# Optimization experiments

Measured on AMD Instinct MI355X. Metric: run time of the kernel, lower is better.

## Reference

```python
import jax, jax.numpy as jnp
import numpy as np

D = 256
H = 16
HD = D // H
N_BIAS = 6
B, E = 8, 1024


def _layernorm(x, g, b, eps=1e-5):
    mu = jnp.mean(x, axis=-1, keepdims=True)
    var = jnp.mean(jnp.square(x - mu), axis=-1, keepdims=True)
    return (x - mu) * jax.lax.rsqrt(var + eps) * g + b


def setup_inputs() -> dict:
    key = jax.random.key(0)
    ks = jax.random.split(key, 16)
    s = 0.02
    inp = {
        "x": jax.random.normal(ks[0], (B, E, D), dtype=jnp.float32),
        "struct_bias": jax.random.randint(ks[1], (B, E, E), 0, N_BIAS),
        "key_padding_mask": jnp.zeros((B, E), dtype=bool),
        # projections stored as [in, out] so y = x @ W + b
        "Wq": jax.random.normal(ks[2], (D, D), jnp.float32) * s,
        "bq": jnp.zeros((D,), jnp.float32),
        "Wk": jax.random.normal(ks[3], (D, D), jnp.float32) * s,
        "bk": jnp.zeros((D,), jnp.float32),
        "Wv": jax.random.normal(ks[4], (D, D), jnp.float32) * s,
        "bv": jnp.zeros((D,), jnp.float32),
        "Wo": jax.random.normal(ks[5], (D, D), jnp.float32) * s,
        "bo": jnp.zeros((D,), jnp.float32),
        "bias_emb": jax.random.normal(ks[6], (N_BIAS, H), jnp.float32) * s,
        "ln1_g": jnp.ones((D,), jnp.float32),
        "ln1_b": jnp.zeros((D,), jnp.float32),
        "W_ff1": jax.random.normal(ks[7], (D, 4 * D), jnp.float32) * s,
        "b_ff1": jnp.zeros((4 * D,), jnp.float32),
        "W_ff2": jax.random.normal(ks[8], (4 * D, D), jnp.float32) * s,
        "b_ff2": jnp.zeros((D,), jnp.float32),
        "ln2_g": jnp.ones((D,), jnp.float32),
        "ln2_b": jnp.zeros((D,), jnp.float32),
    }
    return inp


def reference(x, struct_bias, key_padding_mask, Wq, bq, Wk, bk, Wv, bv, Wo, bo,
              bias_emb, ln1_g, ln1_b, W_ff1, b_ff1, W_ff2, b_ff2, ln2_g, ln2_b):
    b, e, d = x.shape
    # project and split heads: [B, H, E, HD]
    q = (x @ Wq + bq).reshape(b, e, H, HD).transpose(0, 2, 1, 3)
    k = (x @ Wk + bk).reshape(b, e, H, HD).transpose(0, 2, 1, 3)
    v = (x @ Wv + bv).reshape(b, e, H, HD).transpose(0, 2, 1, 3)
    scores = jnp.einsum('bhqd,bhkd->bhqk', q, k) / np.sqrt(HD).astype(np.float32)
    # learned structural bias: [B,E,E,H] -> [B,H,E,E]
    bias = bias_emb[struct_bias].transpose(0, 3, 1, 2)
    scores = scores + bias
    scores = jnp.where(key_padding_mask[:, None, None, :], -jnp.inf, scores)
    attn = jax.nn.softmax(scores, axis=-1)
    out = jnp.einsum('bhqk,bhkd->bhqd', attn, v)
    out = out.transpose(0, 2, 1, 3).reshape(b, e, d)
    out = out @ Wo + bo
    x = _layernorm(x + out, ln1_g, ln1_b)
    ff = jax.nn.gelu(x @ W_ff1 + b_ff1, approximate=False) @ W_ff2 + b_ff2
    x = _layernorm(x + ff, ln2_g, ln2_b)
    return x
```

## Files before the change

### kernel.cpp

```cpp
#include <hip/hip_runtime.h>
#include <math.h>

#define B_  8
#define E_  1024
#define D_  256
#define H_  16
#define FF_ 1024
#define M_  (B_ * E_)

typedef __attribute__((ext_vector_type(8))) short short8;
typedef __attribute__((ext_vector_type(4))) float f32x4;
typedef unsigned short bf16u;

#define GLOAD_LDS16(g, l) __builtin_amdgcn_global_load_lds( \
    (const __attribute__((address_space(1))) void*)(g), \
    (__attribute__((address_space(3))) void*)(l), 16, 0, 0)

__device__ __forceinline__ unsigned short f2bf(float f) {
  union { float f; unsigned u; } c; c.f = f;
  unsigned r = c.u + 0x7fffu + ((c.u >> 16) & 1u);
  return (unsigned short)(r >> 16);
}
__device__ __forceinline__ float gelu_exact(float x) {
  return 0.5f * x * (1.0f + erff(x * 0.70710678118654752f));
}

template<int BM, int BN, int EPI>
__global__ __launch_bounds__(256) void mm_k(
    const bf16u* __restrict__ A, const bf16u* __restrict__ Wt,
    const float* __restrict__ bias, const float* __restrict__ R,
    void* __restrict__ Cout, int M, int N, int K)
{
  constexpr int WM = BM / 2, WN = BN / 2;
  constexpr int MT = WM / 16, NT = WN / 16;
  constexpr int PA = BM * 8 / 256, PB = BN * 8 / 256;
  constexpr int LBM = (BM == 128 ? 7 : 6), LBN = (BN == 128 ? 7 : 6);
  __shared__ bf16u As[BM * 64];
  __shared__ bf16u Bs[BN * 64];

  const int t = threadIdx.x;
  const int l15 = t & 15, quad = (t >> 4) & 3;
  const int w = t >> 6, wm = w >> 1, wn = w & 1;
  const int m0 = blockIdx.x * BM, n0 = blockIdx.y * BN;

  f32x4 acc[MT][NT];
  const f32x4 z4 = {0.f, 0.f, 0.f, 0.f};
#pragma unroll
  for (int i = 0; i < MT; ++i)
#pragma unroll
    for (int j = 0; j < NT; ++j) acc[i][j] = z4;

  for (int k0 = 0; k0 < K; k0 += 64) {
    __syncthreads();
#pragma unroll
    for (int p = 0; p < PA; ++p) {
      int g = p * 256 + t;
      int m = g & (BM - 1), c = g >> LBM;
      const bf16u* src = A + (size_t)(m0 + m) * K + k0 + c * 8;
      GLOAD_LDS16(src, As + g * 8);
    }
#pragma unroll
    for (int p = 0; p < PB; ++p) {
      int g = p * 256 + t;
      int n = g & (BN - 1), c = g >> LBN;
      const bf16u* src = Wt + (size_t)(n0 + n) * K + k0 + c * 8;
      GLOAD_LDS16(src, Bs + g * 8);
    }
    __syncthreads();
#pragma unroll
    for (int s = 0; s < 2; ++s) {
      short8 af[MT], bfr[NT];
#pragma unroll
      for (int mt = 0; mt < MT; ++mt)
        af[mt] = *(const short8*)(As + ((s * 4 + quad) * BM + wm * WM + mt * 16 + l15) * 8);
#pragma unroll
      for (int nt = 0; nt < NT; ++nt)
        bfr[nt] = *(const short8*)(Bs + ((s * 4 + quad) * BN + wn * WN + nt * 16 + l15) * 8);
#pragma unroll
      for (int mt = 0; mt < MT; ++mt)
#pragma unroll
        for (int nt = 0; nt < NT; ++nt)
          acc[mt][nt] = __builtin_amdgcn_mfma_f32_16x16x32_bf16(
              af[mt], bfr[nt], acc[mt][nt], 0, 0, 0);
    }
  }

#pragma unroll
  for (int mt = 0; mt < MT; ++mt) {
#pragma unroll
    for (int nt = 0; nt < NT; ++nt) {
      int col = n0 + wn * WN + nt * 16 + l15;
      float bia = bias[col];
#pragma unroll
      for (int r = 0; r < 4; ++r) {
        int row = m0 + wm * WM + mt * 16 + quad * 4 + r;
        size_t idx = (size_t)row * N + col;
        float v = acc[mt][nt][r] + bia;
        if (EPI == 1)      { ((float*)Cout)[idx] = v + R[idx]; }
        else if (EPI == 2) { ((bf16u*)Cout)[idx] = f2bf(gelu_exact(v)); }
        else               { ((bf16u*)Cout)[idx] = f2bf(v); }
      }
    }
  }
}

__global__ __launch_bounds__(256) void tcvt4_k(
    const float* __restrict__ s0, const float* __restrict__ s1,
    const float* __restrict__ s2, const float* __restrict__ s3,
    bf16u* __restrict__ d0, bf16u* __restrict__ d1,
    bf16u* __restrict__ d2, bf16u* __restrict__ d3)
{
  const int z = blockIdx.z;
  const float* src = (z == 0) ? s0 : (z == 1) ? s1 : (z == 2) ? s2 : s3;
  bf16u* dst = (z == 0) ? d0 : (z == 1) ? d1 : (z == 2) ? d2 : d3;
  __shared__ float tile[32][33];
  const int tx = threadIdx.x & 31, ty = threadIdx.x >> 5;
  const int kb = blockIdx.x * 32, nb = blockIdx.y * 32;
#pragma unroll
  for (int r = 0; r < 4; ++r)
    tile[ty + 8 * r][tx] = src[(size_t)(kb + ty + 8 * r) * 256 + nb + tx];
  __syncthreads();
#pragma unroll
  for (int r = 0; r < 4; ++r)
    dst[(size_t)(nb + ty + 8 * r) * 256 + kb + tx] = f2bf(tile[tx][ty + 8 * r]);
}

__global__ __launch_bounds__(256) void tcvt_k(const float* __restrict__ src,
    bf16u* __restrict__ dst, int K, int N)
{
  __shared__ float tile[32][33];
  const int tx = threadIdx.x & 31, ty = threadIdx.x >> 5;
  const int kb = blockIdx.x * 32, nb = blockIdx.y * 32;
#pragma unroll
  for (int r = 0; r < 4; ++r)
    tile[ty + 8 * r][tx] = src[(size_t)(kb + ty + 8 * r) * N + nb + tx];
  __syncthreads();
#pragma unroll
  for (int r = 0; r < 4; ++r)
    dst[(size_t)(nb + ty + 8 * r) * K + kb + tx] = f2bf(tile[tx][ty + 8 * r]);
}

__global__ __launch_bounds__(256) void cvt_k(const float* __restrict__ X,
    bf16u* __restrict__ Y)
{
  int i = blockIdx.x * 256 + threadIdx.x;
  float4 a = ((const float4*)X)[i * 2];
  float4 b = ((const float4*)X)[i * 2 + 1];
  uint4 o;
  o.x = f2bf(a.x) | ((unsigned)f2bf(a.y) << 16);
  o.y = f2bf(a.z) | ((unsigned)f2bf(a.w) << 16);
  o.z = f2bf(b.x) | ((unsigned)f2bf(b.y) << 16);
  o.w = f2bf(b.z) | ((unsigned)f2bf(b.w) << 16);
  ((uint4*)Y)[i] = o;
}

__global__ void bcat_k(const float* __restrict__ bq, const float* __restrict__ bk,
                       const float* __restrict__ bv, float* __restrict__ o)
{
  int i = blockIdx.x * 256 + threadIdx.x;
  o[i] = (i < 256) ? bq[i] : (i < 512) ? bk[i - 256] : bv[i - 512];
}

__global__ __launch_bounds__(256) void attn_k(
    const bf16u* __restrict__ qkv, const int* __restrict__ sb,
    const unsigned char* __restrict__ mask, const float* __restrict__ be,
    bf16u* __restrict__ O)
{
  __shared__ bf16u Kl[2][64][40];
  __shared__ bf16u Vt[2][16][72];
  __shared__ bf16u Pl[4][16][40];
  __shared__ float embl[2][6];

  const int t    = threadIdx.x;
  const int b    = blockIdx.z;
  const int hg   = blockIdx.y;
  const int w    = t >> 6;
  const int lane = t & 63;
  const int l15  = lane & 15;
  const int quad = lane >> 4;
  const int q0w  = blockIdx.x * 64 + w * 16;

  if (t < 12) embl[t / 6][t % 6] = be[(t % 6) * 16 + hg * 2 + t / 6];

  {
    float4 z = {0.f, 0.f, 0.f, 0.f};
    float4* kp = (float4*)&Kl[0][0][0];
    for (int i = t; i < 640; i += 256) kp[i] = z;
  }

  short8 qf[2];
#pragma unroll
  for (int hp = 0; hp < 2; ++hp) {
    uint4 v = {0u, 0u, 0u, 0u};
    if (quad < 2)
      v = *(const uint4*)(qkv + ((size_t)(b * E_) + q0w + l15) * 768 +
                          (hg * 2 + hp) * 16 + quad * 8);
    else if (quad == 2)
      v.x = 0x3F80u;
    union { uint4 u; short8 s; } c; c.u = v;
    qf[hp] = c.s;
  }

  const int s_hp   = t >> 7;
  const int s_key  = (t >> 1) & 63;
  const int s_half = t & 1;
  const size_t kvbase = (size_t)b * E_ * 768;
  const int* sbp = sb + ((size_t)b * E_ + q0w) * E_;

  f32x4 accO[2];
  const f32x4 z4 = {0.f, 0.f, 0.f, 0.f};
  accO[0] = z4; accO[1] = z4;
  float lsum[2][4] = {};

  for (int k0 = 0; k0 < E_; k0 += 64) {
    int sbv[2][2][4];
#pragma unroll
    for (int s2 = 0; s2 < 2; ++s2)
#pragma unroll
      for (int f = 0; f < 2; ++f)
#pragma unroll
        for (int r = 0; r < 4; ++r)
          sbv[s2][f][r] = sbp[(size_t)(quad * 4 + r) * E_ + k0 + s2 * 32 + f * 16 + l15];

    __syncthreads();
    {
      const bf16u* kq = qkv + kvbase + (size_t)(k0 + s_key) * 768 + 256 +
                        (hg * 2 + s_hp) * 16 + s_half * 8;
      uint4 kw = *(const uint4*)kq;
      uint4 vw = *(const uint4*)(kq + 256);
      *(uint4*)&Kl[s_hp][s_key][s_half * 8] = kw;
      const int col = (s_key >> 5) * 32 + ((s_key & 15) << 1) + ((s_key >> 4) & 1);
      union { uint4 u; bf16u e[8]; } vc; vc.u = vw;
#pragma unroll
      for (int j = 0; j < 8; ++j)
        Vt[s_hp][s_half * 8 + j][col] = vc.e[j];
      if (s_half == 0) {
        unsigned char mv = mask[b * E_ + k0 + s_key];
        Kl[s_hp][s_key][16] = mv ? (bf16u)0xCF6E : (bf16u)0;
      }
    }
    __syncthreads();

#pragma unroll
    for (int hp = 0; hp < 2; ++hp) {
#pragma unroll
      for (int s2 = 0; s2 < 2; ++s2) {
        short8 kf0 = *(const short8*)&Kl[hp][s2 * 32 + l15][quad * 8];
        short8 kf1 = *(const short8*)&Kl[hp][s2 * 32 + 16 + l15][quad * 8];
        f32x4 sc0 = __builtin_amdgcn_mfma_f32_16x16x32_bf16(qf[hp], kf0, z4, 0, 0, 0);
        f32x4 sc1 = __builtin_amdgcn_mfma_f32_16x16x32_bf16(qf[hp], kf1, z4, 0, 0, 0);
#pragma unroll
        for (int r = 0; r < 4; ++r) {
          float w0 = embl[hp][sbv[s2][0][r]];
          float w1 = embl[hp][sbv[s2][1][r]];
          float p0 = __expf(fmaf(sc0[r], 0.25f, w0));
          float p1 = __expf(fmaf(sc1[r], 0.25f, w1));
          unsigned u0 = __float_as_uint(p0) & 0xffff0000u;
          unsigned u1 = __float_as_uint(p1) & 0xffff0000u;
          lsum[hp][r] += __uint_as_float(u0) + __uint_as_float(u1);
          *(unsigned*)&Pl[w][quad * 4 + r][l15 * 2] = (__float_as_uint(p0) >> 16) | u1;
        }
        short8 pf = *(const short8*)&Pl[w][l15][quad * 8];
        short8 vf = *(const short8*)&Vt[hp][l15][s2 * 32 + quad * 8];
        accO[hp] = __builtin_amdgcn_mfma_f32_16x16x32_bf16(pf, vf, accO[hp], 0, 0, 0);
      }
    }
  }

#pragma unroll
  for (int off = 1; off <= 8; off <<= 1)
#pragma unroll
    for (int hp = 0; hp < 2; ++hp)
#pragma unroll
      for (int r = 0; r < 4; ++r)
        lsum[hp][r] += __shfl_xor(lsum[hp][r], off, 64);

#pragma unroll
  for (int hp = 0; hp < 2; ++hp) {
#pragma unroll
    for (int r = 0; r < 4; ++r) {
      float o = accO[hp][r] / lsum[hp][r];
      O[((size_t)(b * E_) + q0w + quad * 4 + r) * 256 + (hg * 2 + hp) * 16 + l15] = f2bf(o);
    }
  }
}

template<int DUAL>
__global__ __launch_bounds__(256) void ln_k(
    const float* __restrict__ X, const float* __restrict__ g,
    const float* __restrict__ bta, float* __restrict__ Y, bf16u* __restrict__ Yb)
{
  const int row  = blockIdx.x * 4 + (threadIdx.x >> 6);
  const int lane = threadIdx.x & 63;
  float4 v = *(const float4*)(X + (size_t)row * D_ + lane * 4);
  float s  = v.x + v.y + v.z + v.w;
  float ss = v.x * v.x + v.y * v.y + v.z * v.z + v.w * v.w;
#pragma unroll
  for (int off = 32; off; off >>= 1) {
    s  += __shfl_xor(s, off, 64);
    ss += __shfl_xor(ss, off, 64);
  }
  float mu  = s * (1.f / 256.f);
  float var = ss * (1.f / 256.f) - mu * mu;
  float rs  = 1.f / sqrtf(var + 1e-5f);
  float4 gv = *(const float4*)(g + lane * 4);
  float4 bv = *(const float4*)(bta + lane * 4);
  float4 o;
  o.x = (v.x - mu) * rs * gv.x + bv.x;
  o.y = (v.y - mu) * rs * gv.y + bv.y;
  o.z = (v.z - mu) * rs * gv.z + bv.z;
  o.w = (v.w - mu) * rs * gv.w + bv.w;
  *(float4*)(Y + (size_t)row * D_ + lane * 4) = o;
  if (DUAL) {
    uint2 p;
    p.x = f2bf(o.x) | ((unsigned)f2bf(o.y) << 16);
    p.y = f2bf(o.z) | ((unsigned)f2bf(o.w) << 16);
    *(uint2*)(Yb + (size_t)row * D_ + lane * 4) = p;
  }
}

extern "C" void kernel_launch(void* const* d_in, const int* in_sizes, int n_in,
                              void* d_out, int out_size, void* d_ws, size_t ws_size,
                              hipStream_t stream) {
  const float* x   = (const float*)d_in[0];
  const int*   sb  = (const int*)d_in[1];
  const unsigned char* mask = (const unsigned char*)d_in[2];
  const float* Wq  = (const float*)d_in[3];
  const float* bq  = (const float*)d_in[4];
  const float* Wk  = (const float*)d_in[5];
  const float* bk  = (const float*)d_in[6];
  const float* Wv  = (const float*)d_in[7];
  const float* bv  = (const float*)d_in[8];
  const float* Wo  = (const float*)d_in[9];
  const float* bo  = (const float*)d_in[10];
  const float* be  = (const float*)d_in[11];
  const float* g1  = (const float*)d_in[12];
  const float* b1  = (const float*)d_in[13];
  const float* Wf1 = (const float*)d_in[14];
  const float* bf1 = (const float*)d_in[15];
  const float* Wf2 = (const float*)d_in[16];
  const float* bf2 = (const float*)d_in[17];
  const float* g2  = (const float*)d_in[18];
  const float* b2  = (const float*)d_in[19];
  float* out = (float*)d_out;

  char* ws = (char*)d_ws;
  bf16u* Wqkvt = (bf16u*)(ws + 0);
  bf16u* Wot   = (bf16u*)(ws + 393216);
  bf16u* Wf1t  = (bf16u*)(ws + 524288);
  bf16u* Wf2t  = (bf16u*)(ws + 1048576);
  float* bqkv  = (float*)(ws + 1572864);
  bf16u* xb    = (bf16u*)(ws + 2097152);
  bf16u* qkv   = (bf16u*)(ws + 6291456);
  bf16u* att   = (bf16u*)(ws + 18874368);
  float* t1    = (float*)(ws + 23068672);
  float* x1    = (float*)(ws + 31457280);
  bf16u* x1b   = (bf16u*)(ws + 39845888);
  bf16u* ffh   = (bf16u*)(ws + 2097152);
  float* t2    = (float*)(ws + 18874368);

  dim3 blk(256);

  tcvt4_k<<<dim3(8, 8, 4), blk, 0, stream>>>(Wq, Wk, Wv, Wo,
      Wqkvt, Wqkvt + 65536, Wqkvt + 131072, Wot);
  tcvt_k<<<dim3(8, 32), blk, 0, stream>>>(Wf1, Wf1t, 256, 1024);
  tcvt_k<<<dim3(32, 8), blk, 0, stream>>>(Wf2, Wf2t, 1024, 256);
  bcat_k<<<3, blk, 0, stream>>>(bq, bk, bv, bqkv);
  cvt_k<<<1024, blk, 0, stream>>>(x, xb);

  mm_k<128, 128, 0><<<dim3(64, 6), blk, 0, stream>>>(xb, Wqkvt, bqkv, nullptr,
                                                     qkv, M_, 768, 256);
  attn_k<<<dim3(16, 8, 8), blk, 0, stream>>>(qkv, sb, mask, be, att);

  mm_k<64, 64, 1><<<dim3(128, 4), blk, 0, stream>>>(att, Wot, bo, x,
                                                    t1, M_, 256, 256);
  ln_k<1><<<M_ / 4, blk, 0, stream>>>(t1, g1, b1, x1, x1b);

  mm_k<128, 128, 2><<<dim3(64, 8), blk, 0, stream>>>(x1b, Wf1t, bf1, nullptr,
                                                     ffh, M_, 1024, 256);
  mm_k<64, 64, 1><<<dim3(128, 4), blk, 0, stream>>>(ffh, Wf2t, bf2, x1,
                                                    t2, M_, 256, 1024);
  ln_k<0><<<M_ / 4, blk, 0, stream>>>(t2, g2, b2, out, nullptr);
}
```

Baseline: 239.5 us.

## Fuse residual+LayerNorm into output GEMMs and merge prep kernels into one launch

Adds a GEMM kernel that computes a full 32-row by 256-column output tile per block, adds bias and residual, and does LayerNorm in the epilogue with a cross-wave reduction in LDS. It replaces the Wo and FF2 GEMMs plus their separate LayerNorm passes, removing the fp32 intermediate round trips and two launches. The five weight, bias and input conversion kernels are also merged into a single prep launch. The fused GEMM uses only 256 blocks with a large B tile and no double-buffering, so it may lose parallelism and latency hiding compared with the previous 512-block GEMMs.

```diff
diff --git a/kernel.cpp b/kernel.cpp
--- a/kernel.cpp
+++ b/kernel.cpp
@@ -96,69 +96,198 @@
         int row = m0 + wm * WM + mt * 16 + quad * 4 + r;
         size_t idx = (size_t)row * N + col;
         float v = acc[mt][nt][r] + bia;
-        if (EPI == 1)      { ((float*)Cout)[idx] = v + R[idx]; }
-        else if (EPI == 2) { ((bf16u*)Cout)[idx] = f2bf(gelu_exact(v)); }
-        else               { ((bf16u*)Cout)[idx] = f2bf(v); }
-      }
-    }
-  }
-}
-
-__global__ __launch_bounds__(256) void tcvt4_k(
-    const float* __restrict__ s0, const float* __restrict__ s1,
-    const float* __restrict__ s2, const float* __restrict__ s3,
-    bf16u* __restrict__ d0, bf16u* __restrict__ d1,
-    bf16u* __restrict__ d2, bf16u* __restrict__ d3)
+        if (EPI == 2) { ((bf16u*)Cout)[idx] = f2bf(gelu_exact(v)); }
+        else          { ((bf16u*)Cout)[idx] = f2bf(v); }
+      }
+    }
+  }
+}
+
+template<int K_, int LN1>
+__global__ __launch_bounds__(256) void mm_ln_k(
+    const bf16u* __restrict__ A, const bf16u* __restrict__ Wt,
+    const float* __restrict__ bias, const float* __restrict__ R,
+    const float* __restrict__ gam, const float* __restrict__ bet,
+    float* __restrict__ Yf, bf16u* __restrict__ Yb)
 {
-  const int z = blockIdx.z;
-  const float* src = (z == 0) ? s0 : (z == 1) ? s1 : (z == 2) ? s2 : s3;
-  bf16u* dst = (z == 0) ? d0 : (z == 1) ? d1 : (z == 2) ? d2 : d3;
-  __shared__ float tile[32][33];
-  const int tx = threadIdx.x & 31, ty = threadIdx.x >> 5;
-  const int kb = blockIdx.x * 32, nb = blockIdx.y * 32;
-#pragma unroll
-  for (int r = 0; r < 4; ++r)
-    tile[ty + 8 * r][tx] = src[(size_t)(kb + ty + 8 * r) * 256 + nb + tx];
+  __shared__ bf16u As[32 * 64];
+  __shared__ bf16u Bs[256 * 64];
+  __shared__ float red[2][32][4];
+
+  const int t = threadIdx.x;
+  const int l15 = t & 15, quad = (t >> 4) & 3;
+  const int w = t >> 6;
+  const int m0 = blockIdx.x * 32;
+
+  f32x4 acc[2][4];
+  const f32x4 z4 = {0.f, 0.f, 0.f, 0.f};
+#pragma unroll
+  for (int i = 0; i < 2; ++i)
+#pragma unroll
+    for (int j = 0; j < 4; ++j) acc[i][j] = z4;
+
+  for (int k0 = 0; k0 < K_; k0 += 64) {
+    __syncthreads();
+    {
+      const bf16u* src = A + (size_t)(m0 + (t & 31)) * K_ + k0 + (t >> 5) * 8;
+      GLOAD_LDS16(src, As + t * 8);
+    }
+#pragma unroll
+    for (int p = 0; p < 8; ++p) {
+      int g = p * 256 + t;
+      const bf16u* src = Wt + (size_t)(g & 255) * K_ + k0 + (g >> 8) * 8;
+      GLOAD_LDS16(src, Bs + g * 8);
+    }
+    __syncthreads();
+#pragma unroll
+    for (int s = 0; s < 2; ++s) {
+      const int cc = s * 4 + quad;
+      short8 af[2], bfr[4];
+#pragma unroll
+      for (int mt = 0; mt < 2; ++mt)
+        af[mt] = *(const short8*)(As + (cc * 32 + mt * 16 + l15) * 8);
+#pragma unroll
+      for (int nt = 0; nt < 4; ++nt)
+        bfr[nt] = *(const short8*)(Bs + (cc * 256 + w * 64 + nt * 16 + l15) * 8);
+#pragma unroll
+      for (int mt = 0; mt < 2; ++mt)
+#pragma unroll
+        for (int nt = 0; nt < 4; ++nt)
+          acc[mt][nt] = __builtin_amdgcn_mfma_f32_16x16x32_bf16(
+              af[mt], bfr[nt], acc[mt][nt], 0, 0, 0);
+    }
+  }
+
+  float ga[4], be4[4], bi[4];
+#pragma unroll
+  for (int nt = 0; nt < 4; ++nt) {
+    int col = w * 64 + nt * 16 + l15;
+    bi[nt] = bias[col]; ga[nt] = gam[col]; be4[nt] = bet[col];
+  }
+#pragma unroll
+  for (int mt = 0; mt < 2; ++mt)
+#pragma unroll
+    for (int nt = 0; nt < 4; ++nt) {
+      int col = w * 64 + nt * 16 + l15;
+#pragma unroll
+      for (int r = 0; r < 4; ++r) {
+        int row = m0 + mt * 16 + quad * 4 + r;
+        acc[mt][nt][r] += bi[nt] + R[(size_t)row * 256 + col];
+      }
+    }
+
+  float s1[2][4], s2[2][4];
+#pragma unroll
+  for (int mt = 0; mt < 2; ++mt)
+#pragma unroll
+    for (int r = 0; r < 4; ++r) {
+      float a = 0.f, b = 0.f;
+#pragma unroll
+      for (int nt = 0; nt < 4; ++nt) {
+        float v = acc[mt][nt][r];
+        a += v; b += v * v;
+      }
+      s1[mt][r] = a; s2[mt][r] = b;
+    }
+#pragma unroll
+  for (int off = 1; off <= 8; off <<= 1)
+#pragma unroll
+    for (int mt = 0; mt < 2; ++mt)
+#pragma unroll
+      for (int r = 0; r < 4; ++r) {
+        s1[mt][r] += __shfl_xor(s1[mt][r], off, 64);
+        s2[mt][r] += __shfl_xor(s2[mt][r], off, 64);
+      }
+  if (l15 == 0) {
+#pragma unroll
+    for (int mt = 0; mt < 2; ++mt)
+#pragma unroll
+      for (int r = 0; r < 4; ++r) {
+        int row32 = mt * 16 + quad * 4 + r;
+        red[0][row32][w] = s1[mt][r];
+        red[1][row32][w] = s2[mt][r];
+      }
+  }
   __syncthreads();
-#pragma unroll
-  for (int r = 0; r < 4; ++r)
-    dst[(size_t)(nb + ty + 8 * r) * 256 + kb + tx] = f2bf(tile[tx][ty + 8 * r]);
-}
-
-__global__ __launch_bounds__(256) void tcvt_k(const float* __restrict__ src,
-    bf16u* __restrict__ dst, int K, int N)
+
+#pragma unroll
+  for (int mt = 0; mt < 2; ++mt)
+#pragma unroll
+    for (int r = 0; r < 4; ++r) {
+      int row32 = mt * 16 + quad * 4 + r;
+      float4 sa = *(const float4*)&red[0][row32][0];
+      float4 sb = *(const float4*)&red[1][row32][0];
+      float sum = sa.x + sa.y + sa.z + sa.w;
+      float sq  = sb.x + sb.y + sb.z + sb.w;
+      float mu  = sum * (1.f / 256.f);
+      float var = sq * (1.f / 256.f) - mu * mu;
+      float rs  = 1.f / sqrtf(var + 1e-5f);
+      int row = m0 + row32;
+#pragma unroll
+      for (int nt = 0; nt < 4; ++nt) {
+        int col = w * 64 + nt * 16 + l15;
+        float y = (acc[mt][nt][r] - mu) * rs * ga[nt] + be4[nt];
+        size_t idx = (size_t)row * 256 + col;
+        Yf[idx] = y;
+        if (LN1) Yb[idx] = f2bf(y);
+      }
+    }
+}
+
+__global__ __launch_bounds__(256) void prep_k(
+    const float* __restrict__ x, bf16u* __restrict__ xb,
+    const float* __restrict__ Wq, const float* __restrict__ Wk,
+    const float* __restrict__ Wv, const float* __restrict__ Wo,
+    bf16u* __restrict__ Wqkvt, bf16u* __restrict__ Wot,
+    const float* __restrict__ Wf1, bf16u* __restrict__ Wf1t,
+    const float* __restrict__ Wf2, bf16u* __restrict__ Wf2t,
+    const float* __restrict__ bq, const float* __restrict__ bk,
+    const float* __restrict__ bv, float* __restrict__ bqkv)
 {
   __shared__ float tile[32][33];
-  const int tx = threadIdx.x & 31, ty = threadIdx.x >> 5;
-  const int kb = blockIdx.x * 32, nb = blockIdx.y * 32;
-#pragma unroll
-  for (int r = 0; r < 4; ++r)
-    tile[ty + 8 * r][tx] = src[(size_t)(kb + ty + 8 * r) * N + nb + tx];
-  __syncthreads();
-#pragma unroll
-  for (int r = 0; r < 4; ++r)
-    dst[(size_t)(nb + ty + 8 * r) * K + kb + tx] = f2bf(tile[tx][ty + 8 * r]);
-}
-
-__global__ __launch_bounds__(256) void cvt_k(const float* __restrict__ X,
-    bf16u* __restrict__ Y)
-{
-  int i = blockIdx.x * 256 + threadIdx.x;
-  float4 a = ((const float4*)X)[i * 2];
-  float4 b = ((const float4*)X)[i * 2 + 1];
-  uint4 o;
-  o.x = f2bf(a.x) | ((unsigned)f2bf(a.y) << 16);
-  o.y = f2bf(a.z) | ((unsigned)f2bf(a.w) << 16);
-  o.z = f2bf(b.x) | ((unsigned)f2bf(b.y) << 16);
-  o.w = f2bf(b.z) | ((unsigned)f2bf(b.w) << 16);
-  ((uint4*)Y)[i] = o;
-}
-
-__global__ void bcat_k(const float* __restrict__ bq, const float* __restrict__ bk,
-                       const float* __restrict__ bv, float* __restrict__ o)
-{
-  int i = blockIdx.x * 256 + threadIdx.x;
-  o[i] = (i < 256) ? bq[i] : (i < 512) ? bk[i - 256] : bv[i - 512];
+  const int bid = blockIdx.x;
+  const int t = threadIdx.x;
+
+  if (bid < 1024) {
+    int i = bid * 256 + t;
+    float4 a = ((const float4*)x)[i * 2];
+    float4 b = ((const float4*)x)[i * 2 + 1];
+    uint4 o;
+    o.x = f2bf(a.x) | ((unsigned)f2bf(a.y) << 16);
+    o.y = f2bf(a.z) | ((unsigned)f2bf(a.w) << 16);
+    o.z = f2bf(b.x) | ((unsigned)f2bf(b.y) << 16);
+    o.w = f2bf(b.z) | ((unsigned)f2bf(b.w) << 16);
+    ((uint4*)xb)[i] = o;
+  } else if (bid < 1792) {
+    const float* src; bf16u* dst; int K, N, kb, nb;
+    int rr = bid - 1024;
+    if (rr < 256) {
+      int z = rr >> 6, i = rr & 63;
+      src = (z == 0) ? Wq : (z == 1) ? Wk : (z == 2) ? Wv : Wo;
+      dst = (z == 0) ? Wqkvt : (z == 1) ? Wqkvt + 65536
+          : (z == 2) ? Wqkvt + 131072 : Wot;
+      K = 256; N = 256; kb = (i & 7) * 32; nb = (i >> 3) * 32;
+    } else if (rr < 512) {
+      int i = rr - 256;
+      src = Wf1; dst = Wf1t; K = 256; N = 1024;
+      kb = (i & 7) * 32; nb = (i >> 3) * 32;
+    } else {
+      int i = rr - 512;
+      src = Wf2; dst = Wf2t; K = 1024; N = 256;
+      kb = (i & 31) * 32; nb = (i >> 5) * 32;
+    }
+    const int tx = t & 31, ty = t >> 5;
+#pragma unroll
+    for (int r = 0; r < 4; ++r)
+      tile[ty + 8 * r][tx] = src[(size_t)(kb + ty + 8 * r) * N + nb + tx];
+    __syncthreads();
+#pragma unroll
+    for (int r = 0; r < 4; ++r)
+      dst[(size_t)(nb + ty + 8 * r) * K + kb + tx] = f2bf(tile[tx][ty + 8 * r]);
+  } else {
+    for (int i = t; i < 768; i += 256)
+      bqkv[i] = (i < 256) ? bq[i] : (i < 512) ? bk[i - 256] : bv[i - 512];
+  }
 }
 
 __global__ __launch_bounds__(256) void attn_k(
@@ -282,40 +411,6 @@
       float o = accO[hp][r] / lsum[hp][r];
       O[((size_t)(b * E_) + q0w + quad * 4 + r) * 256 + (hg * 2 + hp) * 16 + l15] = f2bf(o);
     }
-  }
-}
-
-template<int DUAL>
-__global__ __launch_bounds__(256) void ln_k(
-    const float* __restrict__ X, const float* __restrict__ g,
-    const float* __restrict__ bta, float* __restrict__ Y, bf16u* __restrict__ Yb)
-{
-  const int row  = blockIdx.x * 4 + (threadIdx.x >> 6);
-  const int lane = threadIdx.x & 63;
-  float4 v = *(const float4*)(X + (size_t)row * D_ + lane * 4);
-  float s  = v.x + v.y + v.z + v.w;
-  float ss = v.x * v.x + v.y * v.y + v.z * v.z + v.w * v.w;
-#pragma unroll
-  for (int off = 32; off; off >>= 1) {
-    s  += __shfl_xor(s, off, 64);
-    ss += __shfl_xor(ss, off, 64);
-  }
-  float mu  = s * (1.f / 256.f);
-  float var = ss * (1.f / 256.f) - mu * mu;
-  float rs  = 1.f / sqrtf(var + 1e-5f);
-  float4 gv = *(const float4*)(g + lane * 4);
-  float4 bv = *(const float4*)(bta + lane * 4);
-  float4 o;
-  o.x = (v.x - mu) * rs * gv.x + bv.x;
-  o.y = (v.y - mu) * rs * gv.y + bv.y;
-  o.z = (v.z - mu) * rs * gv.z + bv.z;
-  o.w = (v.w - mu) * rs * gv.w + bv.w;
-  *(float4*)(Y + (size_t)row * D_ + lane * 4) = o;
-  if (DUAL) {
-    uint2 p;
-    p.x = f2bf(o.x) | ((unsigned)f2bf(o.y) << 16);
-    p.y = f2bf(o.z) | ((unsigned)f2bf(o.w) << 16);
-    *(uint2*)(Yb + (size_t)row * D_ + lane * 4) = p;
   }
 }
 
@@ -353,32 +448,22 @@
   bf16u* xb    = (bf16u*)(ws + 2097152);
   bf16u* qkv   = (bf16u*)(ws + 6291456);
   bf16u* att   = (bf16u*)(ws + 18874368);
-  float* t1    = (float*)(ws + 23068672);
-  float* x1    = (float*)(ws + 31457280);
-  bf16u* x1b   = (bf16u*)(ws + 39845888);
+  float* x1    = (float*)(ws + 23068672);
+  bf16u* x1b   = (bf16u*)(ws + 31457280);
   bf16u* ffh   = (bf16u*)(ws + 2097152);
-  float* t2    = (float*)(ws + 18874368);
 
   dim3 blk(256);
 
-  tcvt4_k<<<dim3(8, 8, 4), blk, 0, stream>>>(Wq, Wk, Wv, Wo,
-      Wqkvt, Wqkvt + 65536, Wqkvt + 131072, Wot);
-  tcvt_k<<<dim3(8, 32), blk, 0, stream>>>(Wf1, Wf1t, 256, 1024);
-  tcvt_k<<<dim3(32, 8), blk, 0, stream>>>(Wf2, Wf2t, 1024, 256);
-  bcat_k<<<3, blk, 0, stream>>>(bq, bk, bv, bqkv);
-  cvt_k<<<1024, blk, 0, stream>>>(x, xb);
+  prep_k<<<1793, blk, 0, stream>>>(x, xb, Wq, Wk, Wv, Wo, Wqkvt, Wot,
+                                   Wf1, Wf1t, Wf2, Wf2t, bq, bk, bv, bqkv);
 
   mm_k<128, 128, 0><<<dim3(64, 6), blk, 0, stream>>>(xb, Wqkvt, bqkv, nullptr,
                                                      qkv, M_, 768, 256);
   attn_k<<<dim3(16, 8, 8), blk, 0, stream>>>(qkv, sb, mask, be, att);
 
-  mm_k<64, 64, 1><<<dim3(128, 4), blk, 0, stream>>>(att, Wot, bo, x,
-                                                    t1, M_, 256, 256);
-  ln_k<1><<<M_ / 4, blk, 0, stream>>>(t1, g1, b1, x1, x1b);
+  mm_ln_k<256, 1><<<256, blk, 0, stream>>>(att, Wot, bo, x, g1, b1, x1, x1b);
 
   mm_k<128, 128, 2><<<dim3(64, 8), blk, 0, stream>>>(x1b, Wf1t, bf1, nullptr,
                                                      ffh, M_, 1024, 256);
-  mm_k<64, 64, 1><<<dim3(128, 4), blk, 0, stream>>>(ffh, Wf2t, bf2, x1,
-                                                    t2, M_, 256, 1024);
-  ln_k<0><<<M_ / 4, blk, 0, stream>>>(t2, g2, b2, out, nullptr);
-}
+  mm_ln_k<1024, 0><<<256, blk, 0, stream>>>(ffh, Wf2t, bf2, x1, g2, b2, out, nullptr);
+}
```

After: 243.9 us. No clear change (+1.8%).

## Replace GEMM template with fixed 128x64 tile and 128-deep K blocks

Applied to the files above, without the earlier changes.

Swaps the generic BM/BN GEMM for one kernel with a fixed 128x64 output tile, a K step of 128 and a compile-time K, so the K loop fully unrolls. All four projections use it, which changes grid sizes (more blocks for QKV and FF1, fewer for Wo and FF2). The aim is fewer barrier and load rounds per tile and uniform occupancy. It uses 48KB of LDS per block, which may cut blocks per CU, and the larger tiles for the N=256 GEMMs reduce parallelism.

```diff
diff --git a/kernel.cpp b/kernel.cpp
--- a/kernel.cpp
+++ b/kernel.cpp
@@ -25,75 +25,71 @@
   return 0.5f * x * (1.0f + erff(x * 0.70710678118654752f));
 }
 
-template<int BM, int BN, int EPI>
-__global__ __launch_bounds__(256) void mm_k(
+template<int K_, int EPI>
+__global__ __launch_bounds__(256) void mmrk(
     const bf16u* __restrict__ A, const bf16u* __restrict__ Wt,
     const float* __restrict__ bias, const float* __restrict__ R,
-    void* __restrict__ Cout, int M, int N, int K)
-{
-  constexpr int WM = BM / 2, WN = BN / 2;
-  constexpr int MT = WM / 16, NT = WN / 16;
-  constexpr int PA = BM * 8 / 256, PB = BN * 8 / 256;
-  constexpr int LBM = (BM == 128 ? 7 : 6), LBN = (BN == 128 ? 7 : 6);
-  __shared__ bf16u As[BM * 64];
-  __shared__ bf16u Bs[BN * 64];
+    void* __restrict__ Cout, int N)
+{
+  constexpr int NKB = K_ / 128;
+  __shared__ bf16u As[128 * 128];
+  __shared__ bf16u Bs[64 * 128];
 
   const int t = threadIdx.x;
   const int l15 = t & 15, quad = (t >> 4) & 3;
   const int w = t >> 6, wm = w >> 1, wn = w & 1;
-  const int m0 = blockIdx.x * BM, n0 = blockIdx.y * BN;
-
-  f32x4 acc[MT][NT];
+  const int m0 = blockIdx.x * 128, n0 = blockIdx.y * 64;
+
+  f32x4 acc[4][2];
   const f32x4 z4 = {0.f, 0.f, 0.f, 0.f};
 #pragma unroll
-  for (int i = 0; i < MT; ++i)
-#pragma unroll
-    for (int j = 0; j < NT; ++j) acc[i][j] = z4;
-
-  for (int k0 = 0; k0 < K; k0 += 64) {
+  for (int i = 0; i < 4; ++i) { acc[i][0] = z4; acc[i][1] = z4; }
+
+#pragma unroll
+  for (int kb = 0; kb < NKB; ++kb) {
+    const int k0 = kb * 128;
     __syncthreads();
 #pragma unroll
-    for (int p = 0; p < PA; ++p) {
+    for (int p = 0; p < 8; ++p) {
       int g = p * 256 + t;
-      int m = g & (BM - 1), c = g >> LBM;
-      const bf16u* src = A + (size_t)(m0 + m) * K + k0 + c * 8;
-      GLOAD_LDS16(src, As + g * 8);
-    }
-#pragma unroll
-    for (int p = 0; p < PB; ++p) {
+      int m = g & 127, c = g >> 7;
+      GLOAD_LDS16(A + (size_t)(m0 + m) * K_ + k0 + c * 8, As + g * 8);
+    }
+#pragma unroll
+    for (int p = 0; p < 4; ++p) {
       int g = p * 256 + t;
-      int n = g & (BN - 1), c = g >> LBN;
-      const bf16u* src = Wt + (size_t)(n0 + n) * K + k0 + c * 8;
-      GLOAD_LDS16(src, Bs + g * 8);
+      int n = g & 63, c = g >> 6;
+      GLOAD_LDS16(Wt + (size_t)(n0 + n) * K_ + k0 + c * 8, Bs + g * 8);
     }
     __syncthreads();
 #pragma unroll
-    for (int s = 0; s < 2; ++s) {
-      short8 af[MT], bfr[NT];
-#pragma unroll
-      for (int mt = 0; mt < MT; ++mt)
-        af[mt] = *(const short8*)(As + ((s * 4 + quad) * BM + wm * WM + mt * 16 + l15) * 8);
-#pragma unroll
-      for (int nt = 0; nt < NT; ++nt)
-        bfr[nt] = *(const short8*)(Bs + ((s * 4 + quad) * BN + wn * WN + nt * 16 + l15) * 8);
-#pragma unroll
-      for (int mt = 0; mt < MT; ++mt)
-#pragma unroll
-        for (int nt = 0; nt < NT; ++nt)
+    for (int ks = 0; ks < 4; ++ks) {
+      const int cc = ks * 4 + quad;
+      short8 af[4], bf[2];
+#pragma unroll
+      for (int mt = 0; mt < 4; ++mt)
+        af[mt] = *(const short8*)(As + (cc * 128 + wm * 64 + mt * 16 + l15) * 8);
+#pragma unroll
+      for (int nt = 0; nt < 2; ++nt)
+        bf[nt] = *(const short8*)(Bs + (cc * 64 + wn * 32 + nt * 16 + l15) * 8);
+#pragma unroll
+      for (int mt = 0; mt < 4; ++mt)
+#pragma unroll
+        for (int nt = 0; nt < 2; ++nt)
           acc[mt][nt] = __builtin_amdgcn_mfma_f32_16x16x32_bf16(
-              af[mt], bfr[nt], acc[mt][nt], 0, 0, 0);
-    }
-  }
-
-#pragma unroll
-  for (int mt = 0; mt < MT; ++mt) {
-#pragma unroll
-    for (int nt = 0; nt < NT; ++nt) {
-      int col = n0 + wn * WN + nt * 16 + l15;
+              af[mt], bf[nt], acc[mt][nt], 0, 0, 0);
+    }
+  }
+
+#pragma unroll
+  for (int mt = 0; mt < 4; ++mt) {
+#pragma unroll
+    for (int nt = 0; nt < 2; ++nt) {
+      int col = n0 + wn * 32 + nt * 16 + l15;
       float bia = bias[col];
 #pragma unroll
       for (int r = 0; r < 4; ++r) {
-        int row = m0 + wm * WM + mt * 16 + quad * 4 + r;
+        int row = m0 + wm * 64 + mt * 16 + quad * 4 + r;
         size_t idx = (size_t)row * N + col;
         float v = acc[mt][nt][r] + bia;
         if (EPI == 1)      { ((float*)Cout)[idx] = v + R[idx]; }
@@ -368,17 +364,15 @@
   bcat_k<<<3, blk, 0, stream>>>(bq, bk, bv, bqkv);
   cvt_k<<<1024, blk, 0, stream>>>(x, xb);
 
-  mm_k<128, 128, 0><<<dim3(64, 6), blk, 0, stream>>>(xb, Wqkvt, bqkv, nullptr,
-                                                     qkv, M_, 768, 256);
+  mmrk<256, 0><<<dim3(64, 12), blk, 0, stream>>>(xb, Wqkvt, bqkv, nullptr,
+                                                 qkv, 768);
   attn_k<<<dim3(16, 8, 8), blk, 0, stream>>>(qkv, sb, mask, be, att);
 
-  mm_k<64, 64, 1><<<dim3(128, 4), blk, 0, stream>>>(att, Wot, bo, x,
-                                                    t1, M_, 256, 256);
+  mmrk<256, 1><<<dim3(64, 4), blk, 0, stream>>>(att, Wot, bo, x, t1, 256);
   ln_k<1><<<M_ / 4, blk, 0, stream>>>(t1, g1, b1, x1, x1b);
 
-  mm_k<128, 128, 2><<<dim3(64, 8), blk, 0, stream>>>(x1b, Wf1t, bf1, nullptr,
-                                                     ffh, M_, 1024, 256);
-  mm_k<64, 64, 1><<<dim3(128, 4), blk, 0, stream>>>(ffh, Wf2t, bf2, x1,
-                                                    t2, M_, 256, 1024);
+  mmrk<256, 2><<<dim3(64, 16), blk, 0, stream>>>(x1b, Wf1t, bf1, nullptr,
+                                                 ffh, 1024);
+  mmrk<1024, 1><<<dim3(64, 4), blk, 0, stream>>>(ffh, Wf2t, bf2, x1, t2, 256);
   ln_k<0><<<M_ / 4, blk, 0, stream>>>(t2, g2, b2, out, nullptr);
 }
```

New measurement: 242.7 us. Within noise of the previous version (+1.3%).
